# Performance work log

Hardware: AMD Instinct MI355X
Metric: run time of the kernel (lower is better)

Reference implementation:

```python
import jax, jax.numpy as jnp
import numpy as np

N_NODES = 100000
N_EDGES = 1600000


def _degrees(src, dst, n):
    ones = jnp.ones(src.shape[0], dtype=jnp.float32)
    deg_out = jax.ops.segment_sum(ones, src, num_segments=n)
    deg_in = jax.ops.segment_sum(ones, dst, num_segments=n)
    out_norm = jnp.where(deg_out > 0, jax.lax.rsqrt(jnp.maximum(deg_out, 1.0)), 0.0)
    in_norm = jnp.where(deg_in > 0, jax.lax.rsqrt(jnp.maximum(deg_in, 1.0)), 0.0)
    return out_norm, in_norm


def _graph_conv(h, W, b, src, dst, out_norm, in_norm, act):
    # DGL GraphConv, norm='both': D_out^{-1/2} on src, aggregate, D_in^{-1/2} on dst
    h = h * out_norm[:, None]
    h = h @ W  # project first (in >= out) to shrink edge traffic
    msg = h[src]  # [E, d] gather
    agg = jax.ops.segment_sum(msg, dst, num_segments=h.shape[0])
    agg = agg * in_norm[:, None] + b
    return act(agg) if act is not None else agg


def setup_inputs() -> dict:
    key = jax.random.key(0)
    ks = jax.random.split(key, 8)
    feats = jax.random.normal(ks[0], (N_NODES, 512), dtype=jnp.float32)
    src = jax.random.randint(ks[1], (N_EDGES,), 0, N_NODES)
    dst = jax.random.randint(ks[2], (N_EDGES,), 0, N_NODES)
    W0 = jax.random.normal(ks[3], (512, 256), dtype=jnp.float32) * 0.05
    b0 = jnp.zeros((256,), dtype=jnp.float32)
    Ws = jax.random.normal(ks[4], (5, 256, 256), dtype=jnp.float32) * 0.05
    bs = jnp.zeros((5, 256), dtype=jnp.float32)
    W_out = jax.random.normal(ks[5], (256, 40), dtype=jnp.float32) * 0.05
    b_out = jnp.zeros((40,), dtype=jnp.float32)
    return {"features": feats, "src": src, "dst": dst, "W0": W0, "b0": b0,
            "Ws": Ws, "bs": bs, "W_out": W_out, "b_out": b_out}


def reference(features, src, dst, W0, b0, Ws, bs, W_out, b_out):
    out_norm, in_norm = _degrees(src, dst, features.shape[0])
    act = jax.nn.relu
    # layer 0
    h = _graph_conv(features, W0, b0, src, dst, out_norm, in_norm, act)
    jk = h  # running max over layer outputs (JK max-pool)
    # layers 1..5 (dropout is identity in eval mode)
    for i in range(Ws.shape[0]):
        h = _graph_conv(h, Ws[i], bs[i], src, dst, out_norm, in_norm, act)
        jk = jnp.maximum(jk, h)
    # final GraphConv (no activation) on JK-pooled features, then log_softmax
    h = _graph_conv(jk, W_out, b_out, src, dst, out_norm, in_norm, None)
    return jax.nn.log_softmax(h, axis=1)
```

## Files before the change

### kernel.cpp

```cpp
#include <hip/hip_runtime.h>
#include <hip/hip_bf16.h>
#include <math.h>

#define N_NODES 100000
#define N_EDGES 1600000
#define SCAN_B 1024
#define SCAN_NB ((N_NODES + SCAN_B - 1) / SCAN_B)

typedef _Float16 f16;
typedef f16 f16x8 __attribute__((ext_vector_type(8)));
typedef float f32x4 __attribute__((ext_vector_type(4)));
typedef unsigned short u16;
typedef u16 u16x8 __attribute__((ext_vector_type(8)));
typedef u16 u16x4 __attribute__((ext_vector_type(4)));

__device__ __forceinline__ u16 f16bits(float f) {
  union { f16 h; u16 u; } c; c.h = (f16)f; return c.u;
}
__device__ __forceinline__ float f16val(u16 b) {
  union { u16 u; f16 h; } c; c.u = b; return (float)c.h;
}

__device__ __forceinline__ void gload16(const void* g, void* l) {
  __builtin_amdgcn_global_load_lds(
      (const __attribute__((address_space(1))) void*)g,
      (__attribute__((address_space(3))) void*)l, 16, 0, 0);
}

__device__ __forceinline__ void pair_map(int p, int NBrow, int& row, int& col) {
  int nb = NBrow * 2;
  int cut = (nb >> 4) << 4;
  if (p < cut) { row = ((p >> 4) << 3) + (p & 7); col = (p >> 3) & 1; }
  else { int q = p - cut; row = (cut >> 1) + (q >> 1); col = q & 1; }
}


__global__ void k_count(const int* __restrict__ src, const int* __restrict__ dst,
                        int* __restrict__ deg_out, int* __restrict__ deg_in) {
  int i = blockIdx.x * blockDim.x + threadIdx.x;
  int stride = gridDim.x * blockDim.x;
  for (; i < N_EDGES; i += stride) {
    atomicAdd(&deg_out[src[i]], 1);
    atomicAdd(&deg_in[dst[i]], 1);
  }
}

__global__ void k_norms(const int* __restrict__ deg_out, const int* __restrict__ deg_in,
                        float* __restrict__ norm_out, float* __restrict__ norm_in) {
  int i = blockIdx.x * blockDim.x + threadIdx.x;
  if (i < N_NODES) {
    int a = deg_out[i], b = deg_in[i];
    norm_out[i] = a > 0 ? rsqrtf((float)a) : 0.f;
    norm_in[i]  = b > 0 ? rsqrtf((float)b) : 0.f;
  }
}

__global__ __launch_bounds__(1024) void k_scan1(const int* __restrict__ deg,
                                                int* __restrict__ bsum) {
  __shared__ int red[16];
  int b = blockIdx.x, t = threadIdx.x;
  int i = b * SCAN_B + t;
  int x = (i < N_NODES) ? deg[i] : 0;
#pragma unroll
  for (int o = 32; o > 0; o >>= 1) x += __shfl_down(x, o, 64);
  if ((t & 63) == 0) red[t >> 6] = x;
  __syncthreads();
  if (t == 0) {
    int s = 0;
#pragma unroll
    for (int j = 0; j < 16; ++j) s += red[j];
    bsum[b] = s;
  }
}

__global__ __launch_bounds__(128) void k_scan2(const int* __restrict__ bsum,
                                               int* __restrict__ boffs) {
  __shared__ int buf[128];
  int t = threadIdx.x;
  int x = (t < SCAN_NB) ? bsum[t] : 0;
  buf[t] = x;
  __syncthreads();
  for (int off = 1; off < 128; off <<= 1) {
    int v = (t >= off) ? buf[t - off] : 0;
    __syncthreads();
    buf[t] += v;
    __syncthreads();
  }
  if (t < SCAN_NB) boffs[t] = (t > 0) ? buf[t - 1] : 0;
}

__global__ __launch_bounds__(1024) void k_scan3(const int* __restrict__ deg,
                                                const int* __restrict__ boffs,
                                                int* __restrict__ row_ptr) {
  __shared__ int buf[SCAN_B];
  int b = blockIdx.x, t = threadIdx.x;
  int i = b * SCAN_B + t;
  int x = (i < N_NODES) ? deg[i] : 0;
  buf[t] = x;
  __syncthreads();
  for (int off = 1; off < SCAN_B; off <<= 1) {
    int v = (t >= off) ? buf[t - off] : 0;
    __syncthreads();
    buf[t] += v;
    __syncthreads();
  }
  if (i < N_NODES) row_ptr[i + 1] = boffs[b] + buf[t];
  if (i == 0) row_ptr[0] = 0;
}

__global__ void k_fill(const int* __restrict__ src, const int* __restrict__ dst,
                       const int* __restrict__ row_ptr, int* __restrict__ cursor,
                       int* __restrict__ csr_src) {
  int i = blockIdx.x * blockDim.x + threadIdx.x;
  int stride = gridDim.x * blockDim.x;
  for (; i < N_EDGES; i += stride) {
    int d = dst[i];
    int p = atomicAdd(&cursor[d], 1);
    csr_src[row_ptr[d] + p] = src[i];
  }
}

__global__ void k_wconv(const float* __restrict__ W, int K, int N, int NB,
                        u16* __restrict__ Wt) {
  int i = blockIdx.x * blockDim.x + threadIdx.x;
  if (i >= NB * K) return;
  int col = i / K, k = i - col * K;
  float v = (col < N) ? W[(size_t)k * N + col] : 0.f;
  Wt[i] = f16bits(v);
}


template <int NBCOL, int OUTF32>
__global__ __launch_bounds__(256) void k_gemm_p(
    const u16* __restrict__ Ax, int K,
    const u16* __restrict__ Bx,
    void* __restrict__ Cv, int ldc, int M, int Ncols, int NBrow) {
  __shared__ u16 sA[2][8][4][16][8];
  __shared__ u16 sB[2][8][4][16][8];

  int p = blockIdx.x;
  int row, col;
  if (NBCOL == 2) pair_map(p, NBrow, row, col);
  else { row = p; col = 0; }
  int rowBase = row * 128;
  int colBase = col * 128;

  int t = threadIdx.x;
  int w = t >> 6, l = t & 63;
  int lr = l & 15;
  int kc = l >> 4;

  int gaR0 = min(rowBase + w * 16 + lr, M - 1);
  int gaR1 = min(rowBase + (4 + w) * 16 + lr, M - 1);
  int gbR0 = colBase + w * 16 + lr;
  int gbR1 = colBase + (4 + w) * 16 + lr;

  const u16* pA0 = Ax + (size_t)gaR0 * K + kc * 8;
  const u16* pA1 = Ax + (size_t)gaR1 * K + kc * 8;
  const u16* pB0 = Bx + (size_t)gbR0 * K + kc * 8;
  const u16* pB1 = Bx + (size_t)gbR1 * K + kc * 8;

  int wr = (w >> 1) * 64, wc = (w & 1) * 64;
  int rbA = (w >> 1) * 4;
  int rbB = (w & 1) * 4;
  int crow = kc * 4;

  f32x4 acc[4][4];
#pragma unroll
  for (int r = 0; r < 4; ++r)
#pragma unroll
    for (int c = 0; c < 4; ++c) acc[r][c] = (f32x4)(0.f);

  auto stage = [&](int bb, int k0) {
    gload16(pA0 + k0, &sA[bb][w][0][0][0]);
    gload16(pA1 + k0, &sA[bb][4 + w][0][0][0]);
    gload16(pB0 + k0, &sB[bb][w][0][0][0]);
    gload16(pB1 + k0, &sB[bb][4 + w][0][0][0]);
  };

  int NS = K >> 5;
  stage(0, 0);
  for (int s = 0; s < NS; ++s) {
    int bb = s & 1;
    if (s + 1 < NS) {
      stage(bb ^ 1, (s + 1) * 32);
      asm volatile("s_waitcnt vmcnt(4)" ::: "memory");
    } else {
      asm volatile("s_waitcnt vmcnt(0)" ::: "memory");
    }
    __builtin_amdgcn_s_barrier();

    f16x8 a[4], b[4];
#pragma unroll
    for (int r = 0; r < 4; ++r) a[r] = *(const f16x8*)&sA[bb][rbA + r][kc][lr][0];
#pragma unroll
    for (int c = 0; c < 4; ++c) b[c] = *(const f16x8*)&sB[bb][rbB + c][kc][lr][0];
#pragma unroll
    for (int r = 0; r < 4; ++r)
#pragma unroll
      for (int c = 0; c < 4; ++c)
        acc[r][c] = __builtin_amdgcn_mfma_f32_16x16x32_f16(a[r], b[c], acc[r][c], 0, 0, 0);

    __builtin_amdgcn_s_barrier();
  }

#pragma unroll
  for (int r = 0; r < 4; ++r)
#pragma unroll
    for (int c = 0; c < 4; ++c) {
      int ccol = colBase + wc + c * 16 + lr;
      if (ccol < Ncols) {
#pragma unroll
        for (int j = 0; j < 4; ++j) {
          int rrow = rowBase + wr + r * 16 + crow + j;
          if (rrow < M) {
            if (OUTF32) ((float*)Cv)[(size_t)rrow * ldc + ccol] = acc[r][c][j];
            else        ((u16*)Cv)[(size_t)rrow * ldc + ccol] = f16bits(acc[r][c][j]);
          }
        }
      }
    }
}


__global__ __launch_bounds__(256) void k_gemm_l0(
    const float* __restrict__ Af, int K,
    const u16* __restrict__ Bx,
    const float* __restrict__ rowscale,
    u16* __restrict__ C, int ldc, int M, int Ncols, int NBrow) {
  __shared__ u16 sA[8][4][16][8];
  __shared__ u16 sB[8][4][16][8];

  int row, col;
  pair_map(blockIdx.x, NBrow, row, col);
  int rowBase = row * 128;
  int colBase = col * 128;

  int t = threadIdx.x;
  int w = t >> 6, l = t & 63;
  int lr = l & 15;
  int kc = l >> 4;

  int gaR0 = min(rowBase + w * 16 + lr, M - 1);
  int gaR1 = min(rowBase + (4 + w) * 16 + lr, M - 1);
  int gbR0 = colBase + w * 16 + lr;
  int gbR1 = colBase + (4 + w) * 16 + lr;

  float rs0 = rowscale[gaR0], rs1 = rowscale[gaR1];

  int wr = (w >> 1) * 64, wc = (w & 1) * 64;
  int rbA = (w >> 1) * 4;
  int rbB = (w & 1) * 4;
  int crow = kc * 4;

  f32x4 acc[4][4];
#pragma unroll
  for (int r = 0; r < 4; ++r)
#pragma unroll
    for (int c = 0; c < 4; ++c) acc[r][c] = (f32x4)(0.f);

  for (int k0 = 0; k0 < K; k0 += 32) {
    __syncthreads();
    {
      const float* p0 = Af + (size_t)gaR0 * K + k0 + kc * 8;
      const float* p1 = Af + (size_t)gaR1 * K + k0 + kc * 8;
      float4 v0 = *(const float4*)p0;
      float4 v1 = *(const float4*)(p0 + 4);
      u16x8 h;
      h[0] = f16bits(v0.x * rs0); h[1] = f16bits(v0.y * rs0);
      h[2] = f16bits(v0.z * rs0); h[3] = f16bits(v0.w * rs0);
      h[4] = f16bits(v1.x * rs0); h[5] = f16bits(v1.y * rs0);
      h[6] = f16bits(v1.z * rs0); h[7] = f16bits(v1.w * rs0);
      *(u16x8*)&sA[w][kc][lr][0] = h;
      float4 w0 = *(const float4*)p1;
      float4 w1 = *(const float4*)(p1 + 4);
      h[0] = f16bits(w0.x * rs1); h[1] = f16bits(w0.y * rs1);
      h[2] = f16bits(w0.z * rs1); h[3] = f16bits(w0.w * rs1);
      h[4] = f16bits(w1.x * rs1); h[5] = f16bits(w1.y * rs1);
      h[6] = f16bits(w1.z * rs1); h[7] = f16bits(w1.w * rs1);
      *(u16x8*)&sA[4 + w][kc][lr][0] = h;
    }
    gload16(Bx + (size_t)gbR0 * K + k0 + kc * 8, &sB[w][0][0][0]);
    gload16(Bx + (size_t)gbR1 * K + k0 + kc * 8, &sB[4 + w][0][0][0]);
    __syncthreads();

    f16x8 a[4], b[4];
#pragma unroll
    for (int r = 0; r < 4; ++r) a[r] = *(const f16x8*)&sA[rbA + r][kc][lr][0];
#pragma unroll
    for (int c = 0; c < 4; ++c) b[c] = *(const f16x8*)&sB[rbB + c][kc][lr][0];
#pragma unroll
    for (int r = 0; r < 4; ++r)
#pragma unroll
      for (int c = 0; c < 4; ++c)
        acc[r][c] = __builtin_amdgcn_mfma_f32_16x16x32_f16(a[r], b[c], acc[r][c], 0, 0, 0);
  }

#pragma unroll
  for (int r = 0; r < 4; ++r)
#pragma unroll
    for (int c = 0; c < 4; ++c) {
      int ccol = colBase + wc + c * 16 + lr;
      if (ccol < Ncols) {
#pragma unroll
        for (int j = 0; j < 4; ++j) {
          int rrow = rowBase + wr + r * 16 + crow + j;
          if (rrow < M) C[(size_t)rrow * ldc + ccol] = f16bits(acc[r][c][j]);
        }
      }
    }
}


__global__ __launch_bounds__(256) void k_agg(const u16* __restrict__ proj,
                                             const int* __restrict__ row_ptr,
                                             const int* __restrict__ csr_src,
                                             const float* __restrict__ norm_in,
                                             const float* __restrict__ norm_out,
                                             const float* __restrict__ bias,
                                             u16* __restrict__ hF,
                                             u16* __restrict__ jk, int mode) {
  int wid = __builtin_amdgcn_readfirstlane(threadIdx.x >> 6);
  int node = blockIdx.x * 4 + wid;
  if (node >= N_NODES) return;
  int l4 = (threadIdx.x & 63) * 4;

  int s = row_ptr[node], e = row_ptr[node + 1];
  f32x4 a0 = (f32x4)(0.f), a1 = (f32x4)(0.f), a2 = (f32x4)(0.f), a3 = (f32x4)(0.f);
  int i = s;
  for (; i + 7 < e; i += 8) {
    int u0 = csr_src[i + 0], u1 = csr_src[i + 1], u2 = csr_src[i + 2], u3 = csr_src[i + 3];
    int u4 = csr_src[i + 4], u5 = csr_src[i + 5], u6 = csr_src[i + 6], u7 = csr_src[i + 7];
    u16x4 r0 = *(const u16x4*)(proj + (size_t)u0 * 256 + l4);
    u16x4 r1 = *(const u16x4*)(proj + (size_t)u1 * 256 + l4);
    u16x4 r2 = *(const u16x4*)(proj + (size_t)u2 * 256 + l4);
    u16x4 r3 = *(const u16x4*)(proj + (size_t)u3 * 256 + l4);
    u16x4 r4 = *(const u16x4*)(proj + (size_t)u4 * 256 + l4);
    u16x4 r5 = *(const u16x4*)(proj + (size_t)u5 * 256 + l4);
    u16x4 r6 = *(const u16x4*)(proj + (size_t)u6 * 256 + l4);
    u16x4 r7 = *(const u16x4*)(proj + (size_t)u7 * 256 + l4);
#pragma unroll
    for (int j = 0; j < 4; ++j) {
      a0[j] += f16val(r0[j]) + f16val(r4[j]);
      a1[j] += f16val(r1[j]) + f16val(r5[j]);
      a2[j] += f16val(r2[j]) + f16val(r6[j]);
      a3[j] += f16val(r3[j]) + f16val(r7[j]);
    }
  }
  for (; i + 3 < e; i += 4) {
    int u0 = csr_src[i + 0], u1 = csr_src[i + 1], u2 = csr_src[i + 2], u3 = csr_src[i + 3];
    u16x4 r0 = *(const u16x4*)(proj + (size_t)u0 * 256 + l4);
    u16x4 r1 = *(const u16x4*)(proj + (size_t)u1 * 256 + l4);
    u16x4 r2 = *(const u16x4*)(proj + (size_t)u2 * 256 + l4);
    u16x4 r3 = *(const u16x4*)(proj + (size_t)u3 * 256 + l4);
#pragma unroll
    for (int j = 0; j < 4; ++j) {
      a0[j] += f16val(r0[j]);
      a1[j] += f16val(r1[j]);
      a2[j] += f16val(r2[j]);
      a3[j] += f16val(r3[j]);
    }
  }
  for (; i < e; ++i) {
    u16x4 r0 = *(const u16x4*)(proj + (size_t)csr_src[i] * 256 + l4);
#pragma unroll
    for (int j = 0; j < 4; ++j) a0[j] += f16val(r0[j]);
  }

  float nin = norm_in[node];
  f32x4 b4 = *(const f32x4*)(bias + l4);
  f32x4 v = ((a0 + a1) + (a2 + a3)) * nin + b4;
#pragma unroll
  for (int j = 0; j < 4; ++j) v[j] = fmaxf(v[j], 0.f);

  size_t idx = (size_t)node * 256 + l4;
  f32x4 pv = v;
  if (mode == 0) {
    u16x4 jw;
#pragma unroll
    for (int j = 0; j < 4; ++j) jw[j] = f16bits(v[j]);
    *(u16x4*)(jk + idx) = jw;
  } else {
    u16x4 jold = *(const u16x4*)(jk + idx);
    f32x4 jv;
#pragma unroll
    for (int j = 0; j < 4; ++j) jv[j] = fmaxf(f16val(jold[j]), v[j]);
    if (mode == 1) {
      u16x4 jw;
#pragma unroll
      for (int j = 0; j < 4; ++j) jw[j] = f16bits(jv[j]);
      *(u16x4*)(jk + idx) = jw;
    } else {
      pv = jv;
    }
  }

  float nout = norm_out[node];
  u16x4 hw;
#pragma unroll
  for (int j = 0; j < 4; ++j) hw[j] = f16bits(pv[j] * nout);
  *(u16x4*)(hF + idx) = hw;
}


__global__ __launch_bounds__(64) void k_agg_out(const u16* __restrict__ proj,
                                                const int* __restrict__ row_ptr,
                                                const int* __restrict__ csr_src,
                                                const float* __restrict__ norm_in,
                                                const float* __restrict__ b_out,
                                                float* __restrict__ out) {
  int n = blockIdx.x;
  int c = threadIdx.x;
  int s = row_ptr[n], e = row_ptr[n + 1];
  int cc = (c < 40) ? c : 39;
  float a0 = 0.f, a1 = 0.f, a2 = 0.f, a3 = 0.f;
  int i = s;
  for (; i + 3 < e; i += 4) {
    a0 += f16val(proj[(size_t)csr_src[i] * 40 + cc]);
    a1 += f16val(proj[(size_t)csr_src[i + 1] * 40 + cc]);
    a2 += f16val(proj[(size_t)csr_src[i + 2] * 40 + cc]);
    a3 += f16val(proj[(size_t)csr_src[i + 3] * 40 + cc]);
  }
  for (; i < e; ++i) a0 += f16val(proj[(size_t)csr_src[i] * 40 + cc]);
  float acc = (a0 + a1) + (a2 + a3);
  float v = acc * norm_in[n] + ((c < 40) ? b_out[c] : 0.f);
  float vm = (c < 40) ? v : -3.0e38f;
  float m = vm;
#pragma unroll
  for (int o = 32; o > 0; o >>= 1) m = fmaxf(m, __shfl_xor(m, o, 64));
  float ex = (c < 40) ? __expf(v - m) : 0.f;
  float ssum = ex;
#pragma unroll
  for (int o = 32; o > 0; o >>= 1) ssum += __shfl_xor(ssum, o, 64);
  float lse = m + logf(ssum);
  if (c < 40) out[(size_t)n * 40 + c] = v - lse;
}


extern "C" void kernel_launch(void* const* d_in, const int* in_sizes, int n_in,
                              void* d_out, int out_size, void* d_ws, size_t ws_size,
                              hipStream_t stream) {
  const float* feats = (const float*)d_in[0];
  const int*   src   = (const int*)d_in[1];
  const int*   dst   = (const int*)d_in[2];
  const float* W0    = (const float*)d_in[3];
  const float* b0    = (const float*)d_in[4];
  const float* Ws    = (const float*)d_in[5];
  const float* bs    = (const float*)d_in[6];
  const float* W_out = (const float*)d_in[7];
  const float* b_out = (const float*)d_in[8];
  float* out = (float*)d_out;

  char* base = (char*)d_ws;
  size_t off = 0;
  auto alloc = [&](size_t bytes) -> void* {
    off = (off + 255) & ~(size_t)255;
    void* r = base + off;
    off += bytes;
    return r;
  };
  float* norm_out = (float*)alloc((size_t)N_NODES * 4);
  float* norm_in  = (float*)alloc((size_t)N_NODES * 4);
  int*   deg_out  = (int*)alloc((size_t)N_NODES * 4);
  int*   deg_in   = (int*)alloc((size_t)N_NODES * 4);
  int*   cursor   = (int*)alloc((size_t)N_NODES * 4);
  int*   row_ptr  = (int*)alloc((size_t)(N_NODES + 1) * 4);
  int*   bsum     = (int*)alloc((size_t)SCAN_NB * 4);
  int*   boffs    = (int*)alloc((size_t)SCAN_NB * 4);
  int*   csr_src  = (int*)alloc((size_t)N_EDGES * 4);
  u16*   Wt0      = (u16*)alloc((size_t)256 * 512 * 2);
  u16*   Wts      = (u16*)alloc((size_t)5 * 256 * 256 * 2);
  u16*   Wto      = (u16*)alloc((size_t)128 * 256 * 2);
  u16*   proj40   = (u16*)alloc((size_t)N_NODES * 40 * 2 + 256);
  u16*   hF       = (u16*)alloc((size_t)N_NODES * 256 * 2);
  u16*   bufC     = (u16*)alloc((size_t)N_NODES * 256 * 2);
  u16*   jk       = (u16*)alloc((size_t)N_NODES * 256 * 2);
  (void)ws_size; (void)in_sizes; (void)n_in; (void)out_size;

  hipMemsetAsync(deg_out, 0, (size_t)N_NODES * 4, stream);
  hipMemsetAsync(deg_in,  0, (size_t)N_NODES * 4, stream);
  hipMemsetAsync(cursor,  0, (size_t)N_NODES * 4, stream);

  k_count<<<2048, 256, 0, stream>>>(src, dst, deg_out, deg_in);
  k_norms<<<(N_NODES + 255) / 256, 256, 0, stream>>>(deg_out, deg_in, norm_out, norm_in);
  k_scan1<<<SCAN_NB, 1024, 0, stream>>>(deg_in, bsum);
  k_scan2<<<1, 128, 0, stream>>>(bsum, boffs);
  k_scan3<<<SCAN_NB, 1024, 0, stream>>>(deg_in, boffs, row_ptr);
  k_fill<<<2048, 256, 0, stream>>>(src, dst, row_ptr, cursor, csr_src);

  k_wconv<<<(256 * 512 + 255) / 256, 256, 0, stream>>>(W0, 512, 256, 256, Wt0);
  for (int ll = 0; ll < 5; ++ll)
    k_wconv<<<(256 * 256 + 255) / 256, 256, 0, stream>>>(
        Ws + (size_t)ll * 256 * 256, 256, 256, 256, Wts + (size_t)ll * 256 * 256);
  k_wconv<<<(128 * 256 + 255) / 256, 256, 0, stream>>>(W_out, 256, 40, 128, Wto);

  const int NBROW = (N_NODES + 127) / 128;
  dim3 ga((N_NODES + 3) / 4);
  k_gemm_l0<<<NBROW * 2, 256, 0, stream>>>(feats, 512, Wt0,
                                           norm_out, bufC, 256, N_NODES, 256, NBROW);
  k_agg<<<ga, 256, 0, stream>>>(bufC, row_ptr, csr_src, norm_in, norm_out, b0,
                                hF, jk, 0);
  for (int ll = 0; ll < 5; ++ll) {
    k_gemm_p<2, 0><<<NBROW * 2, 256, 0, stream>>>(hF, 256,
                                                  Wts + (size_t)ll * 256 * 256,
                                                  bufC, 256, N_NODES, 256, NBROW);
    int mode = (ll == 4) ? 2 : 1;
    const float* bias = bs + (size_t)ll * 256;
    k_agg<<<ga, 256, 0, stream>>>(bufC, row_ptr, csr_src, norm_in, norm_out, bias,
                                  hF, jk, mode);
  }
  k_gemm_p<1, 0><<<NBROW, 256, 0, stream>>>(hF, 256, Wto,
                                            proj40, 40, N_NODES, 40, NBROW);
  k_agg_out<<<N_NODES, 64, 0, stream>>>(proj40, row_ptr, csr_src, norm_in, b_out, out);
}
```

Measured before the change: 1.403 ms.

## Deepen GEMM prefetch to triple buffering and register-prefetch fp32 A tiles

The fp16 GEMM moves from double to triple-buffered LDS staging so global loads are issued two k-steps ahead, with vmcnt waits adjusted to match. The fp32-input GEMM now loads the next k-slice of A into registers while the current slice is converted and consumed, using explicit waitcnt and raw barriers in place of __syncthreads. Both changes aim to hide global memory latency behind MFMA work. The cost is extra LDS in the first kernel, possibly lowering occupancy, and more fragile hand-written waitcnt ordering.

Result: no change. 1.407 ms (+0.3%).

```diff
diff --git a/kernel.cpp b/kernel.cpp
--- a/kernel.cpp
+++ b/kernel.cpp
@@ -135,8 +135,8 @@
     const u16* __restrict__ Ax, int K,
     const u16* __restrict__ Bx,
     void* __restrict__ Cv, int ldc, int M, int Ncols, int NBrow) {
-  __shared__ u16 sA[2][8][4][16][8];
-  __shared__ u16 sB[2][8][4][16][8];
+  __shared__ u16 sA[3][8][4][16][8];
+  __shared__ u16 sB[3][8][4][16][8];
 
   int p = blockIdx.x;
   int row, col;
@@ -180,10 +180,13 @@
 
   int NS = K >> 5;
   stage(0, 0);
+  if (1 < NS) stage(1, 32);
   for (int s = 0; s < NS; ++s) {
-    int bb = s & 1;
-    if (s + 1 < NS) {
-      stage(bb ^ 1, (s + 1) * 32);
+    int bb = s % 3;
+    if (s + 2 < NS) {
+      stage((s + 2) % 3, (s + 2) * 32);
+      asm volatile("s_waitcnt vmcnt(8)" ::: "memory");
+    } else if (s + 1 < NS) {
       asm volatile("s_waitcnt vmcnt(4)" ::: "memory");
     } else {
       asm volatile("s_waitcnt vmcnt(0)" ::: "memory");
@@ -246,6 +249,8 @@
   int gbR0 = colBase + w * 16 + lr;
   int gbR1 = colBase + (4 + w) * 16 + lr;
 
+  const float* pA0 = Af + (size_t)gaR0 * K + kc * 8;
+  const float* pA1 = Af + (size_t)gaR1 * K + kc * 8;
   float rs0 = rowscale[gaR0], rs1 = rowscale[gaR1];
 
   int wr = (w >> 1) * 64, wc = (w & 1) * 64;
@@ -259,30 +264,40 @@
 #pragma unroll
     for (int c = 0; c < 4; ++c) acc[r][c] = (f32x4)(0.f);
 
-  for (int k0 = 0; k0 < K; k0 += 32) {
-    __syncthreads();
-    {
-      const float* p0 = Af + (size_t)gaR0 * K + k0 + kc * 8;
-      const float* p1 = Af + (size_t)gaR1 * K + k0 + kc * 8;
-      float4 v0 = *(const float4*)p0;
-      float4 v1 = *(const float4*)(p0 + 4);
-      u16x8 h;
-      h[0] = f16bits(v0.x * rs0); h[1] = f16bits(v0.y * rs0);
-      h[2] = f16bits(v0.z * rs0); h[3] = f16bits(v0.w * rs0);
-      h[4] = f16bits(v1.x * rs0); h[5] = f16bits(v1.y * rs0);
-      h[6] = f16bits(v1.z * rs0); h[7] = f16bits(v1.w * rs0);
-      *(u16x8*)&sA[w][kc][lr][0] = h;
-      float4 w0 = *(const float4*)p1;
-      float4 w1 = *(const float4*)(p1 + 4);
-      h[0] = f16bits(w0.x * rs1); h[1] = f16bits(w0.y * rs1);
-      h[2] = f16bits(w0.z * rs1); h[3] = f16bits(w0.w * rs1);
-      h[4] = f16bits(w1.x * rs1); h[5] = f16bits(w1.y * rs1);
-      h[6] = f16bits(w1.z * rs1); h[7] = f16bits(w1.w * rs1);
-      *(u16x8*)&sA[4 + w][kc][lr][0] = h;
-    }
+  float4 r00 = *(const float4*)(pA0);
+  float4 r01 = *(const float4*)(pA0 + 4);
+  float4 r10 = *(const float4*)(pA1);
+  float4 r11 = *(const float4*)(pA1 + 4);
+
+  int NS = K >> 5;
+  for (int s = 0; s < NS; ++s) {
+    int k0 = s * 32;
+    __builtin_amdgcn_s_barrier();
+    asm volatile("s_waitcnt vmcnt(0)" ::: "memory");
+    u16x8 h;
+    h[0] = f16bits(r00.x * rs0); h[1] = f16bits(r00.y * rs0);
+    h[2] = f16bits(r00.z * rs0); h[3] = f16bits(r00.w * rs0);
+    h[4] = f16bits(r01.x * rs0); h[5] = f16bits(r01.y * rs0);
+    h[6] = f16bits(r01.z * rs0); h[7] = f16bits(r01.w * rs0);
+    *(u16x8*)&sA[w][kc][lr][0] = h;
+    h[0] = f16bits(r10.x * rs1); h[1] = f16bits(r10.y * rs1);
+    h[2] = f16bits(r10.z * rs1); h[3] = f16bits(r10.w * rs1);
+    h[4] = f16bits(r11.x * rs1); h[5] = f16bits(r11.y * rs1);
+    h[6] = f16bits(r11.z * rs1); h[7] = f16bits(r11.w * rs1);
+    *(u16x8*)&sA[4 + w][kc][lr][0] = h;
     gload16(Bx + (size_t)gbR0 * K + k0 + kc * 8, &sB[w][0][0][0]);
     gload16(Bx + (size_t)gbR1 * K + k0 + kc * 8, &sB[4 + w][0][0][0]);
-    __syncthreads();
+    if (s + 1 < NS) {
+      int kn = k0 + 32;
+      r00 = *(const float4*)(pA0 + kn);
+      r01 = *(const float4*)(pA0 + kn + 4);
+      r10 = *(const float4*)(pA1 + kn);
+      r11 = *(const float4*)(pA1 + kn + 4);
+      asm volatile("s_waitcnt vmcnt(4) lgkmcnt(0)" ::: "memory");
+    } else {
+      asm volatile("s_waitcnt vmcnt(0) lgkmcnt(0)" ::: "memory");
+    }
+    __builtin_amdgcn_s_barrier();
 
     f16x8 a[4], b[4];
 #pragma unroll
```
